# Performance work log

Hardware: AMD Instinct MI355X
Metric: run time of the kernel (lower is better)

## Reference

```python
import jax, jax.numpy as jnp
import numpy as np

N = 8192
IN_F = 512
OUT_F = 256
NEG_INF = -9e15
SCORE_DIV = 8.0


def setup_inputs() -> dict:
    key = jax.random.key(0)
    k1, k2, k3, k4 = jax.random.split(key, 4)
    x = jax.random.normal(k1, (N, IN_F), dtype=jnp.float32)
    adj = jax.random.randint(k2, (N, N), 0, 2, dtype=jnp.int32)
    # Xavier-uniform-like params (gain 1.414), as in the torch module
    limW = 1.414 * np.sqrt(6.0 / (IN_F + OUT_F))
    W = jax.random.uniform(k3, (IN_F, OUT_F), dtype=jnp.float32, minval=-limW, maxval=limW)
    lima = 1.414 * np.sqrt(6.0 / (OUT_F + 1))
    a = jax.random.uniform(k4, (OUT_F, 1), dtype=jnp.float32, minval=-lima, maxval=lima)
    return {"input": x, "adj": adj, "W": W, "a": a}


def reference(input, adj, W, a):
    # h: [N, F]
    h = input @ W
    # e[i, j] = sum_k h[i,k] * h[j,k] * a[k]  (equivalent to the repeat/cat/mul path)
    e = (h * a[:, 0]) @ h.T  # [N, N]
    e = jnp.where(adj > 0, e, jnp.float32(NEG_INF))
    attention = jax.nn.softmax(e / SCORE_DIV, axis=1)  # dropout is identity in eval
    h_prime = attention @ h  # [N, F]
    return jax.nn.elu(h_prime)
```

## Files before the change

kernel.cpp:

```cpp
#include <hip/hip_runtime.h>

#define N_ 8192
#define INF_ 512
#define OUTF_ 256
#define KVSPLIT 8
#define BK 32
#define BQ 128
#define NTILES (N_ / KVSPLIT / BK)

typedef float f32x4 __attribute__((ext_vector_type(4)));
typedef float f32x16 __attribute__((ext_vector_type(16)));
typedef __bf16 bf16x8 __attribute__((ext_vector_type(8)));

__device__ __forceinline__ unsigned short f2bf(float f) {
  union { float f; unsigned u; } v; v.f = f;
  unsigned r = v.u + 0x7fffu + ((v.u >> 16) & 1u);
  return (unsigned short)(r >> 16);
}
__device__ __forceinline__ float bf2f(unsigned short u) {
  union { unsigned u; float f; } v; v.u = ((unsigned)u) << 16;
  return v.f;
}

__global__ __launch_bounds__(256) void k_prep(
    const float* __restrict__ x, const float* __restrict__ W,
    unsigned short* __restrict__ xhi, unsigned short* __restrict__ xlo,
    unsigned short* __restrict__ WT)
{
  int idx = blockIdx.x * 256 + threadIdx.x;
  float4 v = ((const float4*)x)[idx];
  float f[4] = {v.x, v.y, v.z, v.w};
  unsigned short h[4], lo[4];
#pragma unroll
  for (int j = 0; j < 4; ++j) {
    h[j] = f2bf(f[j]);
    lo[j] = f2bf(f[j] - bf2f(h[j]));
  }
  *(uint2*)&xhi[idx * 4] = *(uint2*)h;
  *(uint2*)&xlo[idx * 4] = *(uint2*)lo;
  if (idx < INF_ * OUTF_) {
    int c = idx & (OUTF_ - 1);
    int k = idx >> 8;
    WT[c * INF_ + k] = f2bf(W[k * OUTF_ + c]);
  }
}

__global__ __launch_bounds__(256) void k_gemm_h(
    const unsigned short* __restrict__ xhi, const unsigned short* __restrict__ xlo,
    const unsigned short* __restrict__ WT,
    unsigned short* __restrict__ hK, unsigned short* __restrict__ hT)
{
  const int tid = threadIdx.x;
  const int w = tid >> 6, l = tid & 63, g = l >> 4, li = l & 15;
  const int r0 = blockIdx.x * 64 + w * 16;
  const int c0 = blockIdx.y * 64;

  f32x4 acc[4];
  const f32x4 z4 = {0.f, 0.f, 0.f, 0.f};
#pragma unroll
  for (int n = 0; n < 4; ++n) acc[n] = z4;

  const unsigned short* xh = xhi + (size_t)(r0 + li) * INF_ + g * 8;
  const unsigned short* xl = xlo + (size_t)(r0 + li) * INF_ + g * 8;
  const unsigned short* wt = WT + (size_t)(c0 + li) * INF_ + g * 8;

#pragma unroll 4
  for (int kc = 0; kc < 16; ++kc) {
    bf16x8 Ah = *(const bf16x8*)(xh + kc * 32);
    bf16x8 Al = *(const bf16x8*)(xl + kc * 32);
#pragma unroll
    for (int n = 0; n < 4; ++n) {
      bf16x8 Bn = *(const bf16x8*)(wt + (size_t)n * 16 * INF_ + kc * 32);
      acc[n] = __builtin_amdgcn_mfma_f32_16x16x32_bf16(Ah, Bn, acc[n], 0, 0, 0);
      acc[n] = __builtin_amdgcn_mfma_f32_16x16x32_bf16(Al, Bn, acc[n], 0, 0, 0);
    }
  }
#pragma unroll
  for (int n = 0; n < 4; ++n)
#pragma unroll
    for (int s = 0; s < 4; ++s) {
      unsigned short b = f2bf(acc[n][s]);
      int row = r0 + 4 * g + s;
      int col = c0 + n * 16 + li;
      hK[(size_t)row * OUTF_ + col] = b;
      hT[(size_t)col * N_ + row] = b;
    }
}

__global__ __launch_bounds__(256, 2) void k_attn(
    const unsigned short* __restrict__ hK, const unsigned short* __restrict__ hT,
    const int* __restrict__ adj, const float* __restrict__ a,
    unsigned short* __restrict__ Opart, float* __restrict__ lsum)
{
  __shared__ __align__(16) unsigned char smem[65536];
  unsigned char* KA = smem;
  unsigned char* VA = smem + 16384;
  unsigned char* KB = smem + 32768;
  unsigned char* VB = smem + 49152;

  const int tid = threadIdx.x;
  const int w = tid >> 6, l = tid & 63;
  const int q32 = l & 31;
  const int hi = l >> 5;
  const int bid = blockIdx.x;
  const int split = bid & 7;
  const int qblk = (bid >> 3) * BQ;
  const int qrw = qblk + w * 32;
  const int jb = split * (N_ / KVSPLIT);
  const float SCALE = 0.18033688011112042f;

  int offK[4], offV[4];
#pragma unroll
  for (int p = 0; p < 4; ++p) {
    int ch = tid + p * 256;
    int rK = ch >> 5, cK = ch & 31;
    offK[p] = rK * OUTF_ + ((cK ^ (rK & 7)) * 8);
    int dV = ch >> 2, cV = ch & 3;
    offV[p] = dV * N_ + ((cV ^ ((dV ^ (dV >> 2)) & 3)) * 8);
  }
  const int kbase = q32 * 512;
  const int ehk = (hi ^ (q32 & 7)) << 4;
  const int sv = (q32 ^ (q32 >> 2)) & 3;
  const int c0v = (sv & 2) | (hi ^ (sv & 1));
  const int voff0 = q32 * 64 + (c0v << 4);

  const int* adjp = adj + (size_t)(qrw + q32) * N_ + jb + 4 * hi;

  bf16x8 Qf[16];
  {
    const unsigned short* hp = hK + (size_t)(qrw + q32) * OUTF_;
#pragma unroll
    for (int kt = 0; kt < 16; ++kt) {
      const int off = kt * 16 + 8 * hi;
      bf16x8 hv = *(const bf16x8*)(hp + off);
      float4 a0 = *(const float4*)(a + off);
      float4 a1 = *(const float4*)(a + off + 4);
      bf16x8 q;
      q[0] = (__bf16)((float)hv[0] * a0.x);
      q[1] = (__bf16)((float)hv[1] * a0.y);
      q[2] = (__bf16)((float)hv[2] * a0.z);
      q[3] = (__bf16)((float)hv[3] * a0.w);
      q[4] = (__bf16)((float)hv[4] * a1.x);
      q[5] = (__bf16)((float)hv[5] * a1.y);
      q[6] = (__bf16)((float)hv[6] * a1.z);
      q[7] = (__bf16)((float)hv[7] * a1.w);
      Qf[kt] = q;
    }
  }

  f32x16 O[8];
#pragma unroll
  for (int dt = 0; dt < 8; ++dt)
#pragma unroll
    for (int r = 0; r < 16; ++r) O[dt][r] = 0.f;
  float lpv = 0.f;

#define STAGE(tt, Kd, Vd) do { \
    const unsigned short* _hk = hK + (size_t)(jb + (tt) * BK) * OUTF_; \
    const unsigned short* _ht = hT + (jb + (tt) * BK); \
    _Pragma("unroll") \
    for (int p = 0; p < 4; ++p) \
      __builtin_amdgcn_global_load_lds( \
        (const __attribute__((address_space(1))) void*)(_hk + offK[p]), \
        (__attribute__((address_space(3))) void*)((Kd) + (p * 256 + w * 64) * 16), 16, 0, 0); \
    _Pragma("unroll") \
    for (int p = 0; p < 4; ++p) \
      __builtin_amdgcn_global_load_lds( \
        (const __attribute__((address_space(1))) void*)(_ht + offV[p]), \
        (__attribute__((address_space(3))) void*)((Vd) + (p * 256 + w * 64) * 16), 16, 0, 0); \
  } while (0)

  int4 ad[4];
  STAGE(0, KA, VA);
#pragma unroll
  for (int i = 0; i < 4; ++i) ad[i] = *(const int4*)(adjp + i * 8);
  __syncthreads();

#pragma unroll 1
  for (int t = 0; t < NTILES; ++t) {
    const unsigned char* Kc = (t & 1) ? KB : KA;
    const unsigned char* Vc = (t & 1) ? VB : VA;
    unsigned char* Kn = (t & 1) ? KA : KB;
    unsigned char* Vn = (t & 1) ? VA : VB;
    if (t < NTILES - 1) STAGE(t + 1, Kn, Vn);

    f32x16 St;
#pragma unroll
    for (int r = 0; r < 16; ++r) St[r] = 0.f;
#pragma unroll
    for (int kt = 0; kt < 16; ++kt) {
      bf16x8 kf = *(const bf16x8*)(Kc + kbase + ((kt << 5) ^ ehk));
      St = __builtin_amdgcn_mfma_f32_32x32x16_bf16(kf, Qf[kt], St, 0, 0, 0);
    }

    unsigned pk[8];
#pragma unroll
    for (int i = 0; i < 8; ++i) {
      int m0, m1;
      const int4 av = ad[i >> 1];
      if ((i & 1) == 0) { m0 = av.x; m1 = av.y; }
      else             { m0 = av.z; m1 = av.w; }
      float e0 = exp2f(St[2 * i]     * SCALE);
      float e1 = exp2f(St[2 * i + 1] * SCALE);
      float v0 = m0 ? e0 : 0.f;
      float v1 = m1 ? e1 : 0.f;
      lpv += v0 + v1;
      asm("v_cvt_pk_bf16_f32 %0, %1, %2" : "=v"(pk[i]) : "v"(v0), "v"(v1));
    }

    if (t + 1 < NTILES) {
#pragma unroll
      for (int i = 0; i < 4; ++i) ad[i] = *(const int4*)(adjp + (t + 1) * 32 + i * 8);
    }

    bf16x8 Pf[2];
#pragma unroll
    for (int tt = 0; tt < 2; ++tt) {
      unsigned u0 = pk[4 * tt],     u2 = pk[4 * tt + 2];
      unsigned u1 = pk[4 * tt + 1], u3 = pk[4 * tt + 3];
      asm("v_permlane32_swap_b32 %0, %1" : "+v"(u0), "+v"(u2));
      asm("v_permlane32_swap_b32 %0, %1" : "+v"(u1), "+v"(u3));
      union { unsigned u[4]; bf16x8 v; } pu;
      pu.u[0] = u0; pu.u[1] = u1; pu.u[2] = u2; pu.u[3] = u3;
      Pf[tt] = pu.v;
    }

#pragma unroll
    for (int dt = 0; dt < 8; ++dt) {
      bf16x8 v0 = *(const bf16x8*)(Vc + dt * 2048 + voff0);
      bf16x8 v1 = *(const bf16x8*)(Vc + dt * 2048 + (voff0 ^ 32));
      O[dt] = __builtin_amdgcn_mfma_f32_32x32x16_bf16(Pf[0], v0, O[dt], 0, 0, 0);
      O[dt] = __builtin_amdgcn_mfma_f32_32x32x16_bf16(Pf[1], v1, O[dt], 0, 0, 0);
    }

    __syncthreads();
  }
#undef STAGE

  {
    float lfull = lpv + __shfl_xor(lpv, 32);
    if (l < 32)
      lsum[(size_t)split * N_ + qrw + q32] = lfull;
  }
  const size_t ob = (size_t)split * N_ * OUTF_;
#pragma unroll
  for (int dt = 0; dt < 8; ++dt)
#pragma unroll
    for (int r = 0; r < 16; ++r) {
      int q = (r & 3) + 8 * (r >> 2) + 4 * hi;
      Opart[ob + (size_t)(qrw + q) * OUTF_ + dt * 32 + q32] = f2bf(O[dt][r]);
    }
}

__global__ __launch_bounds__(256) void k_combine(
    const unsigned short* __restrict__ Opart, const float* __restrict__ lsum,
    float* __restrict__ out)
{
  int idx = blockIdx.x * 256 + threadIdx.x;
  int row = idx >> 6;
  int c = (idx & 63) * 4;
  float L = 0.f, a0 = 0.f, a1 = 0.f, a2 = 0.f, a3 = 0.f;
#pragma unroll
  for (int s = 0; s < KVSPLIT; ++s) {
    L += lsum[(size_t)s * N_ + row];
    uint2 o = *(const uint2*)(Opart + ((size_t)s * N_ + row) * OUTF_ + c);
    a0 += bf2f((unsigned short)(o.x & 0xffff));
    a1 += bf2f((unsigned short)(o.x >> 16));
    a2 += bf2f((unsigned short)(o.y & 0xffff));
    a3 += bf2f((unsigned short)(o.y >> 16));
  }
  float inv = 1.f / L;
  float r0 = a0 * inv, r1 = a1 * inv, r2 = a2 * inv, r3 = a3 * inv;
  float4 r;
  r.x = r0 > 0.f ? r0 : expm1f(r0);
  r.y = r1 > 0.f ? r1 : expm1f(r1);
  r.z = r2 > 0.f ? r2 : expm1f(r2);
  r.w = r3 > 0.f ? r3 : expm1f(r3);
  *(float4*)(out + (size_t)row * OUTF_ + c) = r;
}

extern "C" void kernel_launch(void* const* d_in, const int* in_sizes, int n_in,
                              void* d_out, int out_size, void* d_ws, size_t ws_size,
                              hipStream_t stream) {
  const float* x  = (const float*)d_in[0];
  const int* adj  = (const int*)d_in[1];
  const float* W  = (const float*)d_in[2];
  const float* a  = (const float*)d_in[3];
  float* out = (float*)d_out;
  char* ws = (char*)d_ws;

  unsigned short* hK = (unsigned short*)(ws);
  unsigned short* hT = (unsigned short*)(ws + (size_t)4 * 1024 * 1024);
  unsigned short* WT = (unsigned short*)(ws + (size_t)8 * 1024 * 1024);
  float* lsum = (float*)(ws + (size_t)9 * 1024 * 1024);
  unsigned short* Opart = (unsigned short*)(ws + (size_t)10 * 1024 * 1024);
  unsigned short* xhi = (unsigned short*)(ws + (size_t)10 * 1024 * 1024);
  unsigned short* xlo = (unsigned short*)(ws + (size_t)18 * 1024 * 1024);

  k_prep<<<(N_ * INF_ / 4) / 256, 256, 0, stream>>>(x, W, xhi, xlo, WT);
  dim3 g1(N_ / 64, OUTF_ / 64);
  k_gemm_h<<<g1, 256, 0, stream>>>(xhi, xlo, WT, hK, hT);
  k_attn<<<(N_ / BQ) * KVSPLIT, 256, 0, stream>>>(hK, hT, adj, a, Opart, lsum);
  k_combine<<<(N_ * 64) / 256, 256, 0, stream>>>(Opart, lsum, out);
}
```

Baseline: 161.1 us.

## Enlarge attention tiles to 256 queries by 64 keys with interleaved softmax and PV

Doubles the query block to 256 rows with 512 threads and the key tile to 64, using 128KB of shared memory per block. Each 32-key half-tile is processed separately, and PV MFMAs are interleaved with the exp/mask work. s_setprio hints are added around the MFMA bursts. The score scale is folded into Q, which removes a multiply per score element. The aim is to halve K/V LDS refills per query and cut barrier count, at the cost of occupancy (one block per CU) and a new V swizzle layout.

New measurement: 210.1 us. 1.3x slower.

```diff
diff --git a/kernel.cpp b/kernel.cpp
--- a/kernel.cpp
+++ b/kernel.cpp
@@ -4,8 +4,8 @@
 #define INF_ 512
 #define OUTF_ 256
 #define KVSPLIT 8
-#define BK 32
-#define BQ 128
+#define BK 64
+#define BQ 256
 #define NTILES (N_ / KVSPLIT / BK)
 
 typedef float f32x4 __attribute__((ext_vector_type(4)));
@@ -87,16 +87,16 @@
     }
 }
 
-__global__ __launch_bounds__(256, 2) void k_attn(
+__global__ __launch_bounds__(512) void k_attn(
     const unsigned short* __restrict__ hK, const unsigned short* __restrict__ hT,
     const int* __restrict__ adj, const float* __restrict__ a,
     unsigned short* __restrict__ Opart, float* __restrict__ lsum)
 {
-  __shared__ __align__(16) unsigned char smem[65536];
+  __shared__ __align__(16) unsigned char smem[131072];
   unsigned char* KA = smem;
-  unsigned char* VA = smem + 16384;
-  unsigned char* KB = smem + 32768;
-  unsigned char* VB = smem + 49152;
+  unsigned char* VA = smem + 32768;
+  unsigned char* KB = smem + 65536;
+  unsigned char* VB = smem + 98304;
 
   const int tid = threadIdx.x;
   const int w = tid >> 6, l = tid & 63;
@@ -112,17 +112,21 @@
   int offK[4], offV[4];
 #pragma unroll
   for (int p = 0; p < 4; ++p) {
-    int ch = tid + p * 256;
+    int ch = tid + p * 512;
     int rK = ch >> 5, cK = ch & 31;
     offK[p] = rK * OUTF_ + ((cK ^ (rK & 7)) * 8);
-    int dV = ch >> 2, cV = ch & 3;
-    offV[p] = dV * N_ + ((cV ^ ((dV ^ (dV >> 2)) & 3)) * 8);
+    int dV = ch >> 3, cV = ch & 7;
+    offV[p] = dV * N_ + ((cV ^ (dV & 7)) * 8);
   }
   const int kbase = q32 * 512;
-  const int ehk = (hi ^ (q32 & 7)) << 4;
-  const int sv = (q32 ^ (q32 >> 2)) & 3;
-  const int c0v = (sv & 2) | (hi ^ (sv & 1));
-  const int voff0 = q32 * 64 + (c0v << 4);
+  const int kswz = (hi ^ (q32 & 7)) << 4;
+  const int vrow = q32 * 128;
+  int vc[2][2];
+#pragma unroll
+  for (int h = 0; h < 2; ++h)
+#pragma unroll
+    for (int tt = 0; tt < 2; ++tt)
+      vc[h][tt] = ((h * 4 + tt * 2 + hi) ^ (q32 & 7)) << 4;
 
   const int* adjp = adj + (size_t)(qrw + q32) * N_ + jb + 4 * hi;
 
@@ -136,14 +140,14 @@
       float4 a0 = *(const float4*)(a + off);
       float4 a1 = *(const float4*)(a + off + 4);
       bf16x8 q;
-      q[0] = (__bf16)((float)hv[0] * a0.x);
-      q[1] = (__bf16)((float)hv[1] * a0.y);
-      q[2] = (__bf16)((float)hv[2] * a0.z);
-      q[3] = (__bf16)((float)hv[3] * a0.w);
-      q[4] = (__bf16)((float)hv[4] * a1.x);
-      q[5] = (__bf16)((float)hv[5] * a1.y);
-      q[6] = (__bf16)((float)hv[6] * a1.z);
-      q[7] = (__bf16)((float)hv[7] * a1.w);
+      q[0] = (__bf16)((float)hv[0] * (a0.x * SCALE));
+      q[1] = (__bf16)((float)hv[1] * (a0.y * SCALE));
+      q[2] = (__bf16)((float)hv[2] * (a0.z * SCALE));
+      q[3] = (__bf16)((float)hv[3] * (a0.w * SCALE));
+      q[4] = (__bf16)((float)hv[4] * (a1.x * SCALE));
+      q[5] = (__bf16)((float)hv[5] * (a1.y * SCALE));
+      q[6] = (__bf16)((float)hv[6] * (a1.z * SCALE));
+      q[7] = (__bf16)((float)hv[7] * (a1.w * SCALE));
       Qf[kt] = q;
     }
   }
@@ -162,12 +166,12 @@
     for (int p = 0; p < 4; ++p) \
       __builtin_amdgcn_global_load_lds( \
         (const __attribute__((address_space(1))) void*)(_hk + offK[p]), \
-        (__attribute__((address_space(3))) void*)((Kd) + (p * 256 + w * 64) * 16), 16, 0, 0); \
+        (__attribute__((address_space(3))) void*)((Kd) + (p * 512 + w * 64) * 16), 16, 0, 0); \
     _Pragma("unroll") \
     for (int p = 0; p < 4; ++p) \
       __builtin_amdgcn_global_load_lds( \
         (const __attribute__((address_space(1))) void*)(_ht + offV[p]), \
-        (__attribute__((address_space(3))) void*)((Vd) + (p * 256 + w * 64) * 16), 16, 0, 0); \
+        (__attribute__((address_space(3))) void*)((Vd) + (p * 512 + w * 64) * 16), 16, 0, 0); \
   } while (0)
 
   int4 ad[4];
@@ -184,55 +188,88 @@
     unsigned char* Vn = (t & 1) ? VA : VB;
     if (t < NTILES - 1) STAGE(t + 1, Kn, Vn);
 
-    f32x16 St;
-#pragma unroll
-    for (int r = 0; r < 16; ++r) St[r] = 0.f;
-#pragma unroll
-    for (int kt = 0; kt < 16; ++kt) {
-      bf16x8 kf = *(const bf16x8*)(Kc + kbase + ((kt << 5) ^ ehk));
-      St = __builtin_amdgcn_mfma_f32_32x32x16_bf16(kf, Qf[kt], St, 0, 0, 0);
-    }
-
-    unsigned pk[8];
-#pragma unroll
-    for (int i = 0; i < 8; ++i) {
-      int m0, m1;
-      const int4 av = ad[i >> 1];
-      if ((i & 1) == 0) { m0 = av.x; m1 = av.y; }
-      else             { m0 = av.z; m1 = av.w; }
-      float e0 = exp2f(St[2 * i]     * SCALE);
-      float e1 = exp2f(St[2 * i + 1] * SCALE);
-      float v0 = m0 ? e0 : 0.f;
-      float v1 = m1 ? e1 : 0.f;
-      lpv += v0 + v1;
-      asm("v_cvt_pk_bf16_f32 %0, %1, %2" : "=v"(pk[i]) : "v"(v0), "v"(v1));
-    }
-
-    if (t + 1 < NTILES) {
-#pragma unroll
-      for (int i = 0; i < 4; ++i) ad[i] = *(const int4*)(adjp + (t + 1) * 32 + i * 8);
-    }
-
-    bf16x8 Pf[2];
-#pragma unroll
-    for (int tt = 0; tt < 2; ++tt) {
-      unsigned u0 = pk[4 * tt],     u2 = pk[4 * tt + 2];
-      unsigned u1 = pk[4 * tt + 1], u3 = pk[4 * tt + 3];
-      asm("v_permlane32_swap_b32 %0, %1" : "+v"(u0), "+v"(u2));
-      asm("v_permlane32_swap_b32 %0, %1" : "+v"(u1), "+v"(u3));
-      union { unsigned u[4]; bf16x8 v; } pu;
-      pu.u[0] = u0; pu.u[1] = u1; pu.u[2] = u2; pu.u[3] = u3;
-      Pf[tt] = pu.v;
-    }
-
-#pragma unroll
-    for (int dt = 0; dt < 8; ++dt) {
-      bf16x8 v0 = *(const bf16x8*)(Vc + dt * 2048 + voff0);
-      bf16x8 v1 = *(const bf16x8*)(Vc + dt * 2048 + (voff0 ^ 32));
-      O[dt] = __builtin_amdgcn_mfma_f32_32x32x16_bf16(Pf[0], v0, O[dt], 0, 0, 0);
-      O[dt] = __builtin_amdgcn_mfma_f32_32x32x16_bf16(Pf[1], v1, O[dt], 0, 0, 0);
-    }
-
+#pragma unroll
+    for (int h = 0; h < 2; ++h) {
+      f32x16 St;
+#pragma unroll
+      for (int r = 0; r < 16; ++r) St[r] = 0.f;
+      const unsigned char* krow = Kc + h * 16384 + kbase;
+      __builtin_amdgcn_s_setprio(1);
+#pragma unroll
+      for (int kt = 0; kt < 16; ++kt) {
+        bf16x8 kf = *(const bf16x8*)(krow + ((kt << 5) ^ kswz));
+        St = __builtin_amdgcn_mfma_f32_32x32x16_bf16(kf, Qf[kt], St, 0, 0, 0);
+      }
+      __builtin_amdgcn_s_setprio(0);
+
+      unsigned pk[8];
+#pragma unroll
+      for (int i = 0; i < 4; ++i) {
+        int m0, m1;
+        const int4 av = ad[i >> 1];
+        if ((i & 1) == 0) { m0 = av.x; m1 = av.y; }
+        else             { m0 = av.z; m1 = av.w; }
+        float e0 = exp2f(St[2 * i]);
+        float e1 = exp2f(St[2 * i + 1]);
+        float v0 = m0 ? e0 : 0.f;
+        float v1 = m1 ? e1 : 0.f;
+        lpv += v0 + v1;
+        asm("v_cvt_pk_bf16_f32 %0, %1, %2" : "=v"(pk[i]) : "v"(v0), "v"(v1));
+      }
+      {
+        unsigned u0 = pk[0], u2 = pk[2], u1 = pk[1], u3 = pk[3];
+        asm("v_permlane32_swap_b32 %0, %1" : "+v"(u0), "+v"(u2));
+        asm("v_permlane32_swap_b32 %0, %1" : "+v"(u1), "+v"(u3));
+        union { unsigned u[4]; bf16x8 v; } pu;
+        pu.u[0] = u0; pu.u[1] = u1; pu.u[2] = u2; pu.u[3] = u3;
+        bf16x8 Pf0 = pu.v;
+        const unsigned char* vb0 = Vc + vrow + vc[h][0];
+        __builtin_amdgcn_s_setprio(1);
+#pragma unroll
+        for (int dt = 0; dt < 8; ++dt) {
+          bf16x8 vf = *(const bf16x8*)(vb0 + dt * 4096);
+          O[dt] = __builtin_amdgcn_mfma_f32_32x32x16_bf16(Pf0, vf, O[dt], 0, 0, 0);
+        }
+        __builtin_amdgcn_s_setprio(0);
+      }
+#pragma unroll
+      for (int i = 4; i < 8; ++i) {
+        int m0, m1;
+        const int4 av = ad[i >> 1];
+        if ((i & 1) == 0) { m0 = av.x; m1 = av.y; }
+        else             { m0 = av.z; m1 = av.w; }
+        float e0 = exp2f(St[2 * i]);
+        float e1 = exp2f(St[2 * i + 1]);
+        float v0 = m0 ? e0 : 0.f;
+        float v1 = m1 ? e1 : 0.f;
+        lpv += v0 + v1;
+        asm("v_cvt_pk_bf16_f32 %0, %1, %2" : "=v"(pk[i]) : "v"(v0), "v"(v1));
+      }
+      {
+        int nh = 2 * t + h + 1;
+        if (nh < 2 * NTILES) {
+#pragma unroll
+          for (int i = 0; i < 4; ++i)
+            ad[i] = *(const int4*)(adjp + nh * 32 + i * 8);
+        }
+      }
+      {
+        unsigned u0 = pk[4], u2 = pk[6], u1 = pk[5], u3 = pk[7];
+        asm("v_permlane32_swap_b32 %0, %1" : "+v"(u0), "+v"(u2));
+        asm("v_permlane32_swap_b32 %0, %1" : "+v"(u1), "+v"(u3));
+        union { unsigned u[4]; bf16x8 v; } pu;
+        pu.u[0] = u0; pu.u[1] = u1; pu.u[2] = u2; pu.u[3] = u3;
+        bf16x8 Pf1 = pu.v;
+        const unsigned char* vb1 = Vc + vrow + vc[h][1];
+        __builtin_amdgcn_s_setprio(1);
+#pragma unroll
+        for (int dt = 0; dt < 8; ++dt) {
+          bf16x8 vf = *(const bf16x8*)(vb1 + dt * 4096);
+          O[dt] = __builtin_amdgcn_mfma_f32_32x32x16_bf16(Pf1, vf, O[dt], 0, 0, 0);
+        }
+        __builtin_amdgcn_s_setprio(0);
+      }
+    }
     __syncthreads();
   }
 #undef STAGE
@@ -300,6 +337,6 @@
   k_prep<<<(N_ * INF_ / 4) / 256, 256, 0, stream>>>(x, W, xhi, xlo, WT);
   dim3 g1(N_ / 64, OUTF_ / 64);
   k_gemm_h<<<g1, 256, 0, stream>>>(xhi, xlo, WT, hK, hT);
-  k_attn<<<(N_ / BQ) * KVSPLIT, 256, 0, stream>>>(hK, hT, adj, a, Opart, lsum);
+  k_attn<<<(N_ / BQ) * KVSPLIT, 512, 0, stream>>>(hK, hT, adj, a, Opart, lsum);
   k_combine<<<(N_ * 64) / 256, 256, 0, stream>>>(Opart, lsum, out);
 }
```

## Fold softmax scale into Q, relax tile barrier, add MFMA priority hints

Applied to the files above, without the earlier changes.

Pre-multiplies the softmax scale into the Q fragments, so the per-score multiply before exp2 is no longer needed. Replaces the per-tile __syncthreads with a custom barrier that waits only until two global loads remain outstanding (vmcnt(2)), fenced with sched_barrier. This aims to avoid draining the just-issued adjacency prefetch. It also raises wave priority around both MFMA loops and splits the row-sum accumulator into two chains to shorten the dependency. The hand-counted vmcnt ties correctness to the exact number and order of issued loads, and scaling before the bf16 rounding slightly changes numerics.

New measurement: 159.6 us. About the same (-0.9%).

```diff
diff --git a/kernel.cpp b/kernel.cpp
--- a/kernel.cpp
+++ b/kernel.cpp
@@ -136,14 +136,14 @@
       float4 a0 = *(const float4*)(a + off);
       float4 a1 = *(const float4*)(a + off + 4);
       bf16x8 q;
-      q[0] = (__bf16)((float)hv[0] * a0.x);
-      q[1] = (__bf16)((float)hv[1] * a0.y);
-      q[2] = (__bf16)((float)hv[2] * a0.z);
-      q[3] = (__bf16)((float)hv[3] * a0.w);
-      q[4] = (__bf16)((float)hv[4] * a1.x);
-      q[5] = (__bf16)((float)hv[5] * a1.y);
-      q[6] = (__bf16)((float)hv[6] * a1.z);
-      q[7] = (__bf16)((float)hv[7] * a1.w);
+      q[0] = (__bf16)((float)hv[0] * (a0.x * SCALE));
+      q[1] = (__bf16)((float)hv[1] * (a0.y * SCALE));
+      q[2] = (__bf16)((float)hv[2] * (a0.z * SCALE));
+      q[3] = (__bf16)((float)hv[3] * (a0.w * SCALE));
+      q[4] = (__bf16)((float)hv[4] * (a1.x * SCALE));
+      q[5] = (__bf16)((float)hv[5] * (a1.y * SCALE));
+      q[6] = (__bf16)((float)hv[6] * (a1.z * SCALE));
+      q[7] = (__bf16)((float)hv[7] * (a1.w * SCALE));
       Qf[kt] = q;
     }
   }
@@ -153,7 +153,7 @@
   for (int dt = 0; dt < 8; ++dt)
 #pragma unroll
     for (int r = 0; r < 16; ++r) O[dt][r] = 0.f;
-  float lpv = 0.f;
+  float lp2[2] = {0.f, 0.f};
 
 #define STAGE(tt, Kd, Vd) do { \
     const unsigned short* _hk = hK + (size_t)(jb + (tt) * BK) * OUTF_; \
@@ -168,6 +168,15 @@
       __builtin_amdgcn_global_load_lds( \
         (const __attribute__((address_space(1))) void*)(_ht + offV[p]), \
         (__attribute__((address_space(3))) void*)((Vd) + (p * 256 + w * 64) * 16), 16, 0, 0); \
+    __builtin_amdgcn_sched_barrier(0);  \
+  } while (0)
+
+#define PIPEBAR() do { \
+    __builtin_amdgcn_sched_barrier(0); \
+    asm volatile("s_waitcnt vmcnt(2)" ::: "memory"); \
+    __builtin_amdgcn_sched_barrier(0); \
+    __builtin_amdgcn_s_barrier(); \
+    __builtin_amdgcn_sched_barrier(0); \
   } while (0)
 
   int4 ad[4];
@@ -187,11 +196,13 @@
     f32x16 St;
 #pragma unroll
     for (int r = 0; r < 16; ++r) St[r] = 0.f;
+    __builtin_amdgcn_s_setprio(1);
 #pragma unroll
     for (int kt = 0; kt < 16; ++kt) {
       bf16x8 kf = *(const bf16x8*)(Kc + kbase + ((kt << 5) ^ ehk));
       St = __builtin_amdgcn_mfma_f32_32x32x16_bf16(kf, Qf[kt], St, 0, 0, 0);
     }
+    __builtin_amdgcn_s_setprio(0);
 
     unsigned pk[8];
 #pragma unroll
@@ -200,11 +211,11 @@
       const int4 av = ad[i >> 1];
       if ((i & 1) == 0) { m0 = av.x; m1 = av.y; }
       else             { m0 = av.z; m1 = av.w; }
-      float e0 = exp2f(St[2 * i]     * SCALE);
-      float e1 = exp2f(St[2 * i + 1] * SCALE);
+      float e0 = exp2f(St[2 * i]);
+      float e1 = exp2f(St[2 * i + 1]);
       float v0 = m0 ? e0 : 0.f;
       float v1 = m1 ? e1 : 0.f;
-      lpv += v0 + v1;
+      lp2[i & 1] += v0 + v1;
       asm("v_cvt_pk_bf16_f32 %0, %1, %2" : "=v"(pk[i]) : "v"(v0), "v"(v1));
     }
 
@@ -225,6 +236,7 @@
       Pf[tt] = pu.v;
     }
 
+    __builtin_amdgcn_s_setprio(1);
 #pragma unroll
     for (int dt = 0; dt < 8; ++dt) {
       bf16x8 v0 = *(const bf16x8*)(Vc + dt * 2048 + voff0);
@@ -232,12 +244,15 @@
       O[dt] = __builtin_amdgcn_mfma_f32_32x32x16_bf16(Pf[0], v0, O[dt], 0, 0, 0);
       O[dt] = __builtin_amdgcn_mfma_f32_32x32x16_bf16(Pf[1], v1, O[dt], 0, 0, 0);
     }
-
-    __syncthreads();
+    __builtin_amdgcn_s_setprio(0);
+
+    PIPEBAR();
   }
 #undef STAGE
+#undef PIPEBAR
 
   {
+    float lpv = lp2[0] + lp2[1];
     float lfull = lpv + __shfl_xor(lpv, 32);
     if (l < 32)
       lsum[(size_t)split * N_ + qrw + q32] = lfull;
```
